# Kernel optimization log

Hardware: AMD Instinct MI355X
Metric: run time of the kernel (lower is better)

Reference implementation:

```python
import jax, jax.numpy as jnp
import numpy as np

D = 768           # input_dim == slot_dim
H, DH = 8, 64     # encoder attention heads / head dim (x-transformers defaults)
INNER = 4 * D     # ff_mult=4 GLU inner dim
EPS = 1e-8
N_ITERS = 3
SCALE = D ** -0.5


def _ln(x, g, b):
    m = jnp.mean(x, axis=-1, keepdims=True)
    v = jnp.var(x, axis=-1, keepdims=True)
    return (x - m) / jnp.sqrt(v + 1e-5) * g + b


def setup_inputs() -> dict:
    key = jax.random.key(0)
    ks = jax.random.split(key, 16)
    w = lambda i, shape, s=0.02: jax.random.normal(ks[i], shape, jnp.float32) * s
    return dict(
        x=jax.random.normal(ks[0], (32, 1024, D), jnp.float32),
        noise=jax.random.normal(ks[1], (32, 16, D), jnp.float32),
        init_mu=jax.random.normal(ks[2], (D,), jnp.float32),
        init_log_sigma=w(3, (D,), 0.05),
        Wk=w(4, (D, D)), Wv=w(5, (D, D)), Wq=w(6, (D, D)),
        ni_g=jnp.ones(D), ni_b=jnp.zeros(D),       # norm_input
        ns_g=jnp.ones(D), ns_b=jnp.zeros(D),       # norm_slots
        nica_g=jnp.ones(D), nica_b=jnp.zeros(D),   # norm_ica
        ln1_g=jnp.ones(D), ln1_b=jnp.zeros(D),     # encoder attn pre-norm
        Wq_a=w(7, (D, H * DH)), Wk_a=w(8, (D, H * DH)),
        Wv_a=w(9, (D, H * DH)), Wo_a=w(10, (H * DH, D)),
        ln2_g=jnp.ones(D), ln2_b=jnp.zeros(D),     # encoder ff pre-norm
        W1=w(11, (D, 2 * INNER)), W2=w(12, (INNER, D)),
        lnf_g=jnp.ones(D), lnf_b=jnp.zeros(D),     # encoder final norm
    )


def _inv_cross_attn(q, k, v):
    # softmax over the SLOT axis (dim i), then renormalize over keys j
    dots = jnp.einsum('bid,bjd->bij', q, k) * SCALE
    attn = jax.nn.softmax(dots, axis=1) + EPS
    attn = attn / jnp.sum(attn, axis=-1, keepdims=True)
    updates = jnp.einsum('bjd,bij->bid', v, attn)
    return updates, attn


def _encoder(h, ln1_g, ln1_b, Wq_a, Wk_a, Wv_a, Wo_a, ln2_g, ln2_b, W1, W2, lnf_g, lnf_b):
    b, n, _ = h.shape
    a = _ln(h, ln1_g, ln1_b)
    q = (a @ Wq_a).reshape(b, n, H, DH)
    k = (a @ Wk_a).reshape(b, n, H, DH)
    v = (a @ Wv_a).reshape(b, n, H, DH)
    scores = jnp.einsum('bihd,bjhd->bhij', q, k) * (DH ** -0.5)
    p = jax.nn.softmax(scores, axis=-1)
    o = jnp.einsum('bhij,bjhd->bihd', p, v).reshape(b, n, H * DH)
    h = h + o @ Wo_a
    f = _ln(h, ln2_g, ln2_b)
    u, g = jnp.split(f @ W1, 2, axis=-1)
    h = h + (u * jax.nn.silu(g)) @ W2
    return _ln(h, lnf_g, lnf_b)


def reference(x, noise, init_mu, init_log_sigma, Wk, Wv, Wq,
              ni_g, ni_b, ns_g, ns_b, nica_g, nica_b,
              ln1_g, ln1_b, Wq_a, Wk_a, Wv_a, Wo_a,
              ln2_g, ln2_b, W1, W2, lnf_g, lnf_b):
    xn = _ln(x, ni_g, ni_b)
    k = xn @ Wk
    v = xn @ Wv
    slots = init_mu + jnp.exp(init_log_sigma) * noise  # [b, n_slots, d]

    def step(slots):
        q = _ln(slots, ns_g, ns_b) @ Wq
        updates, attn = _inv_cross_attn(q, k, v)
        slots = _ln(slots + updates, nica_g, nica_b)
        slots = _encoder(slots, ln1_g, ln1_b, Wq_a, Wk_a, Wv_a, Wo_a,
                         ln2_g, ln2_b, W1, W2, lnf_g, lnf_b)
        return slots, attn

    for _ in range(N_ITERS):
        slots, _ = step(slots)
    slots, attn = step(slots)
    attn_map = jnp.transpose(attn, (0, 2, 1))  # b n hw -> b hw n
    return slots, attn_map
```

## Files before the change

### kernel.cpp

```cpp
#include <hip/hip_runtime.h>
#include <hip/hip_bf16.h>
#include <stdint.h>

typedef _Float16 f16;
typedef __attribute__((ext_vector_type(8))) _Float16 f16x8;
typedef __attribute__((ext_vector_type(4))) _Float16 f16x4;
typedef __attribute__((ext_vector_type(4))) float f32x4;

#define GLOBAL_AS __attribute__((address_space(1)))
#define LDS_AS __attribute__((address_space(3)))

#define D_DIM 768
#define NTOK 1024
#define NSLOT 16
#define NB 32
#define NTOT (NB*NTOK)
#define HDIM 512
#define INNER 3072
#define SCALE_D 0.03608439182435161f
#define SCALE_H 0.125f

template<int OUT>
__global__ __launch_bounds__(256) void mgemm64_k(
    const f16* __restrict__ A, const f16* __restrict__ Bt,
    void* __restrict__ Cout, int M, int N, int K, int Kc)
{
  __shared__ __align__(16) f16 As[64*256];
  __shared__ __align__(16) f16 Bs[64*256];
  const int tid = threadIdx.x;
  const int lane = tid & 63;
  const int wave = tid >> 6;
  const int m0 = blockIdx.x*64, n0 = blockIdx.y*64;
  const int kbeg = blockIdx.z * Kc;
  const int wm = (wave>>1)*32, wn = (wave&1)*32;
  const int quad = lane>>4, l16 = lane&15;

  const int sr = tid>>2;
  const int sc = (tid&3)*8;
  const f16* gA = A  + (size_t)(m0+sr)*K + kbeg + sc;
  const f16* gB = Bt + (size_t)(n0+sr)*K + kbeg + sc;
  LDS_AS f16* lA = (LDS_AS f16*)&As[(size_t)tid*8];
  LDS_AS f16* lB = (LDS_AS f16*)&Bs[(size_t)tid*8];

  const f16* fA0 = &As[(wm + l16)*32 + quad*8];
  const f16* fB0 = &Bs[(wn + l16)*32 + quad*8];

  f32x4 acc[2][2] = {};

  for (int k0 = 0; k0 < Kc; k0 += 256){
    #pragma unroll
    for (int p=0;p<8;++p){
      __builtin_amdgcn_global_load_lds((const GLOBAL_AS void*)(gA + k0 + p*32),
                                       (LDS_AS void*)(lA + (size_t)p*2048), 16, 0, 0);
      __builtin_amdgcn_global_load_lds((const GLOBAL_AS void*)(gB + k0 + p*32),
                                       (LDS_AS void*)(lB + (size_t)p*2048), 16, 0, 0);
    }
    __syncthreads();
    #pragma unroll
    for (int p=0;p<8;++p){
      f16x8 a0 = *(const f16x8*)(fA0 + p*2048);
      f16x8 a1 = *(const f16x8*)(fA0 + p*2048 + 16*32);
      f16x8 b0 = *(const f16x8*)(fB0 + p*2048);
      f16x8 b1 = *(const f16x8*)(fB0 + p*2048 + 16*32);
      acc[0][0] = __builtin_amdgcn_mfma_f32_16x16x32_f16(a0,b0,acc[0][0],0,0,0);
      acc[0][1] = __builtin_amdgcn_mfma_f32_16x16x32_f16(a0,b1,acc[0][1],0,0,0);
      acc[1][0] = __builtin_amdgcn_mfma_f32_16x16x32_f16(a1,b0,acc[1][0],0,0,0);
      acc[1][1] = __builtin_amdgcn_mfma_f32_16x16x32_f16(a1,b1,acc[1][1],0,0,0);
    }
    __syncthreads();
  }
  #pragma unroll
  for (int mt=0;mt<2;++mt){
    #pragma unroll
    for (int nt=0;nt<2;++nt){
      int gm = m0 + wm + mt*16 + quad*4;
      int gn = n0 + wn + nt*16 + l16;
      #pragma unroll
      for (int r=0;r<4;++r){
        float c = acc[mt][nt][r];
        size_t idx = (size_t)(gm+r)*N + gn;
        if (OUT==0)      ((float*)Cout)[idx] = c;
        else if (OUT==1) ((f16*)Cout)[idx] = (f16)c;
        else             atomicAdd(&((float*)Cout)[idx], c);
      }
    }
  }
}

__global__ __launch_bounds__(256) void w1glu_k(
    const f16* __restrict__ A, const f16* __restrict__ W1T,
    f16* __restrict__ act, int M)
{
  __shared__ __align__(16) f16 As[64*128];
  __shared__ __align__(16) f16 Bu[64*128];
  __shared__ __align__(16) f16 Bg[64*128];
  const int K = 768;
  const int tid = threadIdx.x;
  const int lane = tid & 63;
  const int wave = tid >> 6;
  const int m0 = blockIdx.x*64, n0 = blockIdx.y*64;
  const int wm = (wave>>1)*32, wn = (wave&1)*32;
  const int quad = lane>>4, l16 = lane&15;

  const int sr = tid>>2;
  const int sc = (tid&3)*8;
  const f16* gA  = A   + (size_t)(m0+sr)*K + sc;
  const f16* gBu = W1T + (size_t)(n0+sr)*K + sc;
  const f16* gBg = W1T + (size_t)(3072+n0+sr)*K + sc;
  LDS_AS f16* lA  = (LDS_AS f16*)&As[(size_t)tid*8];
  LDS_AS f16* lBu = (LDS_AS f16*)&Bu[(size_t)tid*8];
  LDS_AS f16* lBg = (LDS_AS f16*)&Bg[(size_t)tid*8];

  const f16* fA0 = &As[(wm + l16)*32 + quad*8];
  const f16* fU0 = &Bu[(wn + l16)*32 + quad*8];
  const f16* fG0 = &Bg[(wn + l16)*32 + quad*8];

  f32x4 accU[2][2] = {};
  f32x4 accG[2][2] = {};

  for (int k0 = 0; k0 < K; k0 += 128){
    #pragma unroll
    for (int p=0;p<4;++p){
      __builtin_amdgcn_global_load_lds((const GLOBAL_AS void*)(gA  + k0 + p*32),
                                       (LDS_AS void*)(lA  + (size_t)p*2048), 16, 0, 0);
      __builtin_amdgcn_global_load_lds((const GLOBAL_AS void*)(gBu + k0 + p*32),
                                       (LDS_AS void*)(lBu + (size_t)p*2048), 16, 0, 0);
      __builtin_amdgcn_global_load_lds((const GLOBAL_AS void*)(gBg + k0 + p*32),
                                       (LDS_AS void*)(lBg + (size_t)p*2048), 16, 0, 0);
    }
    __syncthreads();
    #pragma unroll
    for (int p=0;p<4;++p){
      f16x8 a0 = *(const f16x8*)(fA0 + p*2048);
      f16x8 a1 = *(const f16x8*)(fA0 + p*2048 + 16*32);
      f16x8 u0 = *(const f16x8*)(fU0 + p*2048);
      f16x8 u1 = *(const f16x8*)(fU0 + p*2048 + 16*32);
      f16x8 g0 = *(const f16x8*)(fG0 + p*2048);
      f16x8 g1 = *(const f16x8*)(fG0 + p*2048 + 16*32);
      accU[0][0] = __builtin_amdgcn_mfma_f32_16x16x32_f16(a0,u0,accU[0][0],0,0,0);
      accU[0][1] = __builtin_amdgcn_mfma_f32_16x16x32_f16(a0,u1,accU[0][1],0,0,0);
      accU[1][0] = __builtin_amdgcn_mfma_f32_16x16x32_f16(a1,u0,accU[1][0],0,0,0);
      accU[1][1] = __builtin_amdgcn_mfma_f32_16x16x32_f16(a1,u1,accU[1][1],0,0,0);
      accG[0][0] = __builtin_amdgcn_mfma_f32_16x16x32_f16(a0,g0,accG[0][0],0,0,0);
      accG[0][1] = __builtin_amdgcn_mfma_f32_16x16x32_f16(a0,g1,accG[0][1],0,0,0);
      accG[1][0] = __builtin_amdgcn_mfma_f32_16x16x32_f16(a1,g0,accG[1][0],0,0,0);
      accG[1][1] = __builtin_amdgcn_mfma_f32_16x16x32_f16(a1,g1,accG[1][1],0,0,0);
    }
    __syncthreads();
  }
  #pragma unroll
  for (int mt=0;mt<2;++mt){
    #pragma unroll
    for (int nt=0;nt<2;++nt){
      int gm = m0 + wm + mt*16 + quad*4;
      int gn = n0 + wn + nt*16 + l16;
      #pragma unroll
      for (int r=0;r<4;++r){
        float u = accU[mt][nt][r];
        float g = accG[mt][nt][r];
        float sg = g / (1.0f + __expf(-g));
        act[(size_t)(gm+r)*INNER + gn] = (f16)(u*sg);
      }
    }
  }
}

__global__ __launch_bounds__(256) void dots_k(
    const f16* __restrict__ Q,
    const f16* __restrict__ Xn,
    f16* __restrict__ attn,
    float* __restrict__ rsPart)
{
  __shared__ __align__(16) f16 qf[16*768];
  __shared__ __align__(16) f16 ks[64*256];
  __shared__ float rpart[4][16];
  const int b = blockIdx.x, jt = blockIdx.y;
  const int tid = threadIdx.x;
  const int lane = tid & 63;
  const int w = tid >> 6;
  const int quad = lane>>4, l16 = lane&15;

  #pragma unroll
  for (int c=0;c<6;++c){
    int p = c*256 + tid;
    int ki = p >> 6, qd = (p >> 4) & 3, rw = p & 15;
    f16x8 v = *(const f16x8*)(Q + ((size_t)(b*NSLOT+rw))*D_DIM + ki*32 + qd*8);
    *(f16x8*)&qf[(size_t)p*8] = v;
  }

  const f16* gK = Xn + ((size_t)(b*NTOK + jt*64 + (tid>>2)))*D_DIM + (tid&3)*8;
  LDS_AS f16* lK = (LDS_AS f16*)&ks[(size_t)tid*8];

  f32x4 acc = {};
  for (int it=0; it<3; ++it){
    #pragma unroll
    for (int p=0;p<8;++p)
      __builtin_amdgcn_global_load_lds((const GLOBAL_AS void*)(gK + it*256 + p*32),
                                       (LDS_AS void*)(lK + (size_t)p*2048), 16, 0, 0);
    __syncthreads();
    #pragma unroll
    for (int p=0;p<8;++p){
      f16x8 a  = *(const f16x8*)&qf[(((size_t)(it*8+p)*4 + quad)*16 + l16)*8];
      f16x8 bf = *(const f16x8*)&ks[(size_t)p*2048 + (w*16+l16)*32 + quad*8];
      acc = __builtin_amdgcn_mfma_f32_16x16x32_f16(a, bf, acc, 0, 0, 0);
    }
    __syncthreads();
  }

  float v0 = acc[0]*SCALE_D, v1 = acc[1]*SCALE_D, v2 = acc[2]*SCALE_D, v3 = acc[3]*SCALE_D;
  float mx = fmaxf(fmaxf(v0,v1), fmaxf(v2,v3));
  mx = fmaxf(mx, __shfl_xor(mx, 16));
  mx = fmaxf(mx, __shfl_xor(mx, 32));
  float e0 = __expf(v0-mx), e1 = __expf(v1-mx), e2 = __expf(v2-mx), e3 = __expf(v3-mx);
  float s = e0+e1+e2+e3;
  s += __shfl_xor(s, 16);
  s += __shfl_xor(s, 32);
  float inv = 1.0f/s;
  float a0 = e0*inv + 1e-8f, a1 = e1*inv + 1e-8f, a2 = e2*inv + 1e-8f, a3 = e3*inv + 1e-8f;

  int jcol = jt*64 + w*16 + l16;
  int ibase = b*NSLOT + quad*4;
  attn[(size_t)(ibase+0)*NTOK + jcol] = (f16)a0;
  attn[(size_t)(ibase+1)*NTOK + jcol] = (f16)a1;
  attn[(size_t)(ibase+2)*NTOK + jcol] = (f16)a2;
  attn[(size_t)(ibase+3)*NTOK + jcol] = (f16)a3;

  float t0=a0, t1=a1, t2=a2, t3=a3;
  #pragma unroll
  for (int m=1;m<16;m<<=1){
    t0 += __shfl_xor(t0, m);
    t1 += __shfl_xor(t1, m);
    t2 += __shfl_xor(t2, m);
    t3 += __shfl_xor(t3, m);
  }
  if (l16 == 0){
    rpart[w][quad*4+0] = t0;
    rpart[w][quad*4+1] = t1;
    rpart[w][quad*4+2] = t2;
    rpart[w][quad*4+3] = t3;
  }
  __syncthreads();
  if (tid < 16){
    float ss = rpart[0][tid] + rpart[1][tid] + rpart[2][tid] + rpart[3][tid];
    rsPart[(size_t)((b*16 + jt)<<4) + tid] = ss;
  }
}

__global__ __launch_bounds__(256) void attnv_k(
    const f16* __restrict__ attn,
    const float* __restrict__ rsPart,
    const f16* __restrict__ XnT,
    f16* __restrict__ t_out)
{
  __shared__ __align__(16) f16 Asl[16*256];
  __shared__ __align__(16) f16 Bsl[64*256];
  __shared__ float rsum[16];
  const int b = blockIdx.x, d0 = blockIdx.y*64;
  const int tid = threadIdx.x;
  const int lane = tid & 63;
  const int w = tid >> 6;
  const int quad = lane>>4, l16 = lane&15;

  if (tid < 16){
    float s = 0.f;
    #pragma unroll
    for (int jt=0;jt<16;++jt) s += rsPart[(size_t)((b*16 + jt)<<4) + tid];
    rsum[tid] = s;
  }

  const int pa = tid>>6, ta = tid&63;
  const f16* gA = attn + ((size_t)(b*NSLOT + (ta>>2)))*NTOK + (ta&3)*8;
  const f16* gB = XnT + ((size_t)(d0 + (tid>>2)))*NTOT + b*NTOK + (tid&3)*8;
  LDS_AS f16* lB = (LDS_AS f16*)&Bsl[(size_t)tid*8];

  f32x4 acc = {};
  for (int it=0; it<4; ++it){
    #pragma unroll
    for (int q=0;q<2;++q){
      int pq = pa*2 + q;
      __builtin_amdgcn_global_load_lds((const GLOBAL_AS void*)(gA + it*256 + pq*32),
                                       (LDS_AS void*)((LDS_AS f16*)&Asl[(size_t)pq*512 + ta*8]), 16, 0, 0);
    }
    #pragma unroll
    for (int p=0;p<8;++p)
      __builtin_amdgcn_global_load_lds((const GLOBAL_AS void*)(gB + it*256 + p*32),
                                       (LDS_AS void*)(lB + (size_t)p*2048), 16, 0, 0);
    __syncthreads();
    #pragma unroll
    for (int p=0;p<8;++p){
      f16x8 a  = *(const f16x8*)&Asl[(size_t)p*512 + l16*32 + quad*8];
      f16x8 bf = *(const f16x8*)&Bsl[(size_t)p*2048 + (w*16+l16)*32 + quad*8];
      acc = __builtin_amdgcn_mfma_f32_16x16x32_f16(a, bf, acc, 0, 0, 0);
    }
    __syncthreads();
  }
  int dcol = d0 + w*16 + l16;
  #pragma unroll
  for (int r=0;r<4;++r){
    int i = quad*4 + r;
    t_out[(size_t)(b*NSLOT + i)*D_DIM + dcol] = (f16)(acc[r] / rsum[i]);
  }
}

__global__ __launch_bounds__(256) void lnw_k(
    const float* __restrict__ X,
    const float* __restrict__ g, const float* __restrict__ bb,
    f16* __restrict__ out)
{
  const int lane = threadIdx.x & 63;
  const size_t row = (size_t)blockIdx.x*4 + (threadIdx.x>>6);
  const float* x = X + row*D_DIM;
  float4 v[3]; float s=0.f, ss=0.f;
  #pragma unroll
  for (int t=0;t<3;++t){
    v[t] = *(const float4*)(x + lane*4 + t*256);
    s  += v[t].x+v[t].y+v[t].z+v[t].w;
    ss += v[t].x*v[t].x+v[t].y*v[t].y+v[t].z*v[t].z+v[t].w*v[t].w;
  }
  #pragma unroll
  for (int m=1;m<64;m<<=1){ s += __shfl_xor(s,m); ss += __shfl_xor(ss,m); }
  float mean = s*(1.0f/768.0f);
  float inv  = rsqrtf(ss*(1.0f/768.0f) - mean*mean + 1e-5f);
  #pragma unroll
  for (int t=0;t<3;++t){
    int c0 = lane*4 + t*256;
    float4 gg = *(const float4*)(g + c0);
    float4 bv = *(const float4*)(bb + c0);
    f16x4 h4;
    h4.x = (f16)((v[t].x-mean)*inv*gg.x + bv.x);
    h4.y = (f16)((v[t].y-mean)*inv*gg.y + bv.y);
    h4.z = (f16)((v[t].z-mean)*inv*gg.z + bv.z);
    h4.w = (f16)((v[t].w-mean)*inv*gg.w + bv.w);
    *(f16x4*)(out + row*D_DIM + c0) = h4;
  }
}

template<bool ADD>
__global__ __launch_bounds__(256) void lnlnw_k(
    const float* __restrict__ X, const float* __restrict__ X2,
    const float* __restrict__ g1, const float* __restrict__ b1,
    const float* __restrict__ g2, const float* __restrict__ b2,
    float* __restrict__ out1, f16* __restrict__ out2)
{
  const int lane = threadIdx.x & 63;
  const size_t row = (size_t)blockIdx.x*4 + (threadIdx.x>>6);
  const float* x = X + row*D_DIM;
  const float* x2 = X2 + row*D_DIM;
  float4 v[3]; float s=0.f, ss=0.f;
  #pragma unroll
  for (int t=0;t<3;++t){
    int c0 = lane*4 + t*256;
    float4 a = *(const float4*)(x + c0);
    if (ADD){
      float4 b = *(const float4*)(x2 + c0);
      a.x+=b.x; a.y+=b.y; a.z+=b.z; a.w+=b.w;
    }
    v[t]=a;
    s  += v[t].x+v[t].y+v[t].z+v[t].w;
    ss += v[t].x*v[t].x+v[t].y*v[t].y+v[t].z*v[t].z+v[t].w*v[t].w;
  }
  #pragma unroll
  for (int m=1;m<64;m<<=1){ s += __shfl_xor(s,m); ss += __shfl_xor(ss,m); }
  float mean = s*(1.0f/768.0f);
  float inv  = rsqrtf(ss*(1.0f/768.0f) - mean*mean + 1e-5f);
  float y[3][4]; float s2=0.f, ss2=0.f;
  #pragma unroll
  for (int t=0;t<3;++t){
    int c0 = lane*4 + t*256;
    float4 gg = *(const float4*)(g1 + c0);
    float4 bv = *(const float4*)(b1 + c0);
    y[t][0] = (v[t].x-mean)*inv*gg.x + bv.x;
    y[t][1] = (v[t].y-mean)*inv*gg.y + bv.y;
    y[t][2] = (v[t].z-mean)*inv*gg.z + bv.z;
    y[t][3] = (v[t].w-mean)*inv*gg.w + bv.w;
    float4 o = { y[t][0], y[t][1], y[t][2], y[t][3] };
    *(float4*)(out1 + row*D_DIM + c0) = o;
    s2  += y[t][0]+y[t][1]+y[t][2]+y[t][3];
    ss2 += y[t][0]*y[t][0]+y[t][1]*y[t][1]+y[t][2]*y[t][2]+y[t][3]*y[t][3];
  }
  #pragma unroll
  for (int m=1;m<64;m<<=1){ s2 += __shfl_xor(s2,m); ss2 += __shfl_xor(ss2,m); }
  float mean2 = s2*(1.0f/768.0f);
  float inv2  = rsqrtf(ss2*(1.0f/768.0f) - mean2*mean2 + 1e-5f);
  #pragma unroll
  for (int t=0;t<3;++t){
    int c0 = lane*4 + t*256;
    float4 gg = *(const float4*)(g2 + c0);
    float4 bv = *(const float4*)(b2 + c0);
    f16x4 h4;
    h4.x = (f16)((y[t][0]-mean2)*inv2*gg.x + bv.x);
    h4.y = (f16)((y[t][1]-mean2)*inv2*gg.y + bv.y);
    h4.z = (f16)((y[t][2]-mean2)*inv2*gg.z + bv.z);
    h4.w = (f16)((y[t][3]-mean2)*inv2*gg.w + bv.w);
    *(f16x4*)(out2 + row*D_DIM + c0) = h4;
  }
}

__global__ __launch_bounds__(256) void slotsinit_k(
    const float* __restrict__ noise, const float* __restrict__ mu,
    const float* __restrict__ ls,
    const float* __restrict__ nsg, const float* __restrict__ nsb,
    float* __restrict__ slots, f16* __restrict__ tmp2)
{
  const int lane = threadIdx.x & 63;
  const size_t row = (size_t)blockIdx.x*4 + (threadIdx.x>>6);
  float4 v[3]; float s=0.f, ss=0.f;
  #pragma unroll
  for (int t=0;t<3;++t){
    int c0 = lane*4 + t*256;
    float4 nz = *(const float4*)(noise + row*D_DIM + c0);
    float4 m4 = *(const float4*)(mu + c0);
    float4 l4 = *(const float4*)(ls + c0);
    v[t].x = m4.x + __expf(l4.x)*nz.x;
    v[t].y = m4.y + __expf(l4.y)*nz.y;
    v[t].z = m4.z + __expf(l4.z)*nz.z;
    v[t].w = m4.w + __expf(l4.w)*nz.w;
    *(float4*)(slots + row*D_DIM + c0) = v[t];
    s  += v[t].x+v[t].y+v[t].z+v[t].w;
    ss += v[t].x*v[t].x+v[t].y*v[t].y+v[t].z*v[t].z+v[t].w*v[t].w;
  }
  #pragma unroll
  for (int m=1;m<64;m<<=1){ s += __shfl_xor(s,m); ss += __shfl_xor(ss,m); }
  float mean = s*(1.0f/768.0f);
  float inv  = rsqrtf(ss*(1.0f/768.0f) - mean*mean + 1e-5f);
  #pragma unroll
  for (int t=0;t<3;++t){
    int c0 = lane*4 + t*256;
    float4 gg = *(const float4*)(nsg + c0);
    float4 bv = *(const float4*)(nsb + c0);
    f16x4 h4;
    h4.x = (f16)((v[t].x-mean)*inv*gg.x + bv.x);
    h4.y = (f16)((v[t].y-mean)*inv*gg.y + bv.y);
    h4.z = (f16)((v[t].z-mean)*inv*gg.z + bv.z);
    h4.w = (f16)((v[t].w-mean)*inv*gg.w + bv.w);
    *(f16x4*)(tmp2 + row*D_DIM + c0) = h4;
  }
}

__global__ __launch_bounds__(256) void encattn_k(
    const f16* __restrict__ QA, const f16* __restrict__ KA,
    const f16* __restrict__ VA, int QSTR,
    f16* __restrict__ O)
{
  __shared__ float qs[16][68], ks[16][68], vs[16][68], ps[16][20];
  const int b = blockIdx.x, h = blockIdx.y;
  const int tid = threadIdx.x;
  {
    int i = tid>>4, dd=(tid&15)*4;
    size_t base = ((size_t)(b*NSLOT+i))*QSTR + h*64 + dd;
    f16x4 uq = *(const f16x4*)(QA + base);
    f16x4 uk = *(const f16x4*)(KA + base);
    f16x4 uv = *(const f16x4*)(VA + base);
    float4 fq = { (float)uq.x, (float)uq.y, (float)uq.z, (float)uq.w };
    float4 fk = { (float)uk.x, (float)uk.y, (float)uk.z, (float)uk.w };
    float4 fv = { (float)uv.x, (float)uv.y, (float)uv.z, (float)uv.w };
    *(float4*)&qs[i][dd]=fq; *(float4*)&ks[i][dd]=fk; *(float4*)&vs[i][dd]=fv;
  }
  __syncthreads();
  {
    int i = tid>>4, j = tid&15;
    float s=0.f;
    #pragma unroll 8
    for (int d=0; d<64; ++d) s += qs[i][d]*ks[j][d];
    ps[i][j] = s*SCALE_H;
  }
  __syncthreads();
  if (tid < 16){
    int i = tid;
    float mx=-1e30f;
    #pragma unroll
    for (int j=0;j<16;++j) mx = fmaxf(mx, ps[i][j]);
    float sm=0.f;
    #pragma unroll
    for (int j=0;j<16;++j){ float e=__expf(ps[i][j]-mx); ps[i][j]=e; sm+=e; }
    float inv=1.0f/sm;
    #pragma unroll
    for (int j=0;j<16;++j) ps[i][j]*=inv;
  }
  __syncthreads();
  {
    int i = tid>>4, dq=(tid&15)*4;
    float a0=0,a1=0,a2=0,a3=0;
    #pragma unroll
    for (int j=0;j<16;++j){
      float p = ps[i][j];
      a0+=p*vs[j][dq+0]; a1+=p*vs[j][dq+1]; a2+=p*vs[j][dq+2]; a3+=p*vs[j][dq+3];
    }
    size_t base = ((size_t)(b*NSLOT+i))*HDIM + h*64 + dq;
    O[base+0]=(f16)a0; O[base+1]=(f16)a1; O[base+2]=(f16)a2; O[base+3]=(f16)a3;
  }
}

__global__ __launch_bounds__(256) void transp_k(
    const f16* __restrict__ in, f16* __restrict__ out, int R, int C)
{
  __shared__ f16 T[64][72];
  const int m0 = blockIdx.x*64, d0 = blockIdx.y*64;
  const int tid = threadIdx.x;
  {
    int r = tid>>2, c = (tid&3)*16;
    const f16* p = in + (size_t)(m0+r)*C + d0 + c;
    *(f16x8*)&T[r][c]   = *(const f16x8*)p;
    *(f16x8*)&T[r][c+8] = *(const f16x8*)(p+8);
  }
  __syncthreads();
  {
    int dd = tid>>2, mq = (tid&3)*16;
    f16 v[16];
    #pragma unroll
    for (int e=0;e<16;++e) v[e] = T[mq+e][dd];
    f16* p = out + (size_t)(d0+dd)*R + m0 + mq;
    *(f16x8*)p     = *(f16x8*)&v[0];
    *(f16x8*)(p+8) = *(f16x8*)&v[8];
  }
}

__global__ __launch_bounds__(256) void prep_k(
    const float* __restrict__ Wv,   const float* __restrict__ Wq_a,
    const float* __restrict__ Wk_a, const float* __restrict__ Wv_a,
    const float* __restrict__ Wo_a, const float* __restrict__ W1,
    const float* __restrict__ W2,   const float* __restrict__ Wk,
    const float* __restrict__ Wq,
    f16* __restrict__ WvT, f16* __restrict__ WqkvT, f16* __restrict__ WoaT,
    f16* __restrict__ W1T, f16* __restrict__ W2T,
    f16* __restrict__ Wkf, f16* __restrict__ Wqf)
{
  __shared__ float t[32][33];
  int bid = blockIdx.x;
  const float* src; f16* dst; int R, C; bool tr = true;
  if      (bid < 576)  {              src=Wv;   dst=WvT;             R=768;  C=768; }
  else if (bid < 960)  { bid-=576;    src=Wq_a; dst=WqkvT;           R=768;  C=512; }
  else if (bid < 1344) { bid-=960;    src=Wk_a; dst=WqkvT+512*768;   R=768;  C=512; }
  else if (bid < 1728) { bid-=1344;   src=Wv_a; dst=WqkvT+1024*768;  R=768;  C=512; }
  else if (bid < 2112) { bid-=1728;   src=Wo_a; dst=WoaT;            R=512;  C=768; }
  else if (bid < 6720) { bid-=2112;   src=W1;   dst=W1T;             R=768;  C=6144; }
  else if (bid < 9024) { bid-=6720;   src=W2;   dst=W2T;             R=3072; C=768; }
  else if (bid < 9600) { bid-=9024;   src=Wk;   dst=Wkf;             R=768;  C=768; tr=false; }
  else                 { bid-=9600;   src=Wq;   dst=Wqf;             R=768;  C=768; tr=false; }
  const int tpr = C/32;
  const int r0 = (bid / tpr)*32, c0 = (bid % tpr)*32;
  const int lc = threadIdx.x & 31, g8 = threadIdx.x >> 5;
  if (tr){
    #pragma unroll
    for (int s=0;s<4;++s){
      int r = g8*4 + s;
      t[r][lc] = src[(size_t)(r0+r)*C + c0+lc];
    }
    __syncthreads();
    #pragma unroll
    for (int s=0;s<4;++s){
      int c = g8*4 + s;
      dst[(size_t)(c0+c)*R + r0+lc] = (f16)t[lc][c];
    }
  } else {
    #pragma unroll
    for (int s=0;s<4;++s){
      int r = g8*4 + s;
      dst[(size_t)(r0+r)*C + c0+lc] = (f16)src[(size_t)(r0+r)*C + c0+lc];
    }
  }
}

__global__ __launch_bounds__(256) void attnout_k(
    const f16* __restrict__ attn, const float* __restrict__ rsPart,
    float* __restrict__ out)
{
  __shared__ float rsum[16];
  const int bid = blockIdx.x, tid = threadIdx.x;
  const int b = bid >> 6;
  if (tid < 16){
    float s = 0.f;
    #pragma unroll
    for (int jt=0;jt<16;++jt) s += rsPart[(size_t)((b*16+jt)<<4) + tid];
    rsum[tid] = s;
  }
  __syncthreads();
  int idx = bid*256 + tid;
  int i = idx & 15;
  int j = (idx >> 4) & 1023;
  out[idx] = (float)attn[((size_t)(b*NSLOT)+i)*NTOK + j] / rsum[i];
}

extern "C" void kernel_launch(void* const* d_in, const int* in_sizes, int n_in,
                              void* d_out, int out_size, void* d_ws, size_t ws_size,
                              hipStream_t stream) {
  const float* x        = (const float*)d_in[0];
  const float* noise    = (const float*)d_in[1];
  const float* init_mu  = (const float*)d_in[2];
  const float* init_ls  = (const float*)d_in[3];
  const float* Wk       = (const float*)d_in[4];
  const float* Wv       = (const float*)d_in[5];
  const float* Wq       = (const float*)d_in[6];
  const float* ni_g     = (const float*)d_in[7];
  const float* ni_b     = (const float*)d_in[8];
  const float* ns_g     = (const float*)d_in[9];
  const float* ns_b     = (const float*)d_in[10];
  const float* nica_g   = (const float*)d_in[11];
  const float* nica_b   = (const float*)d_in[12];
  const float* ln1_g    = (const float*)d_in[13];
  const float* ln1_b    = (const float*)d_in[14];
  const float* Wq_a     = (const float*)d_in[15];
  const float* Wk_a     = (const float*)d_in[16];
  const float* Wv_a     = (const float*)d_in[17];
  const float* Wo_a     = (const float*)d_in[18];
  const float* ln2_g    = (const float*)d_in[19];
  const float* ln2_b    = (const float*)d_in[20];
  const float* W1       = (const float*)d_in[21];
  const float* W2       = (const float*)d_in[22];
  const float* lnf_g    = (const float*)d_in[23];
  const float* lnf_b    = (const float*)d_in[24];

  char* w = (char*)d_ws;
  size_t off = 0;
  auto alloc = [&](size_t bytes)->char*{
    char* p = w + off; off += (bytes + 255) & ~(size_t)255; return p;
  };
  f16* xn_h  = (f16*)alloc((size_t)NTOT*D_DIM*2);
  f16* xnT_h = (f16*)alloc((size_t)D_DIM*NTOT*2);
  f16* Wkf   = (f16*)alloc((size_t)768*768*2);
  f16* Wqf   = (f16*)alloc((size_t)768*768*2);
  f16* BtQK  = (f16*)alloc((size_t)768*768*2);
  f16* WvT   = (f16*)alloc((size_t)768*768*2);
  f16* WqkvT = (f16*)alloc((size_t)1536*768*2);
  f16* WoaT  = (f16*)alloc((size_t)768*512*2);
  f16* W1T   = (f16*)alloc((size_t)6144*768*2);
  f16* W2T   = (f16*)alloc((size_t)768*3072*2);
  float* slots = (float*)alloc(512*768*4);
  float* hbuf  = (float*)alloc(512*768*4);
  float* upd   = (float*)alloc(512*768*4);
  f16* tmp_h  = (f16*)alloc(512*768*2);
  f16* tmp2_h = (f16*)alloc(512*768*2);
  f16* q_h    = (f16*)alloc(512*768*2);
  f16* t_h    = (f16*)alloc(512*768*2);
  f16* qkv_h  = (f16*)alloc((size_t)512*1536*2);
  f16* o_h    = (f16*)alloc(512*512*2);
  f16* act_h  = (f16*)alloc((size_t)512*3072*2);
  f16* attn_h = (f16*)alloc((size_t)NB*NSLOT*NTOK*2);
  float* rsPart = (float*)alloc((size_t)32*16*16*4);

  prep_k<<<10176, 256, 0, stream>>>(Wv, Wq_a, Wk_a, Wv_a, Wo_a, W1, W2, Wk, Wq,
                                    WvT, WqkvT, WoaT, W1T, W2T, Wkf, Wqf);

  mgemm64_k<1><<<dim3(12, 12, 1), 256, 0, stream>>>(Wkf, Wqf, BtQK, 768, 768, 768, 768);

  lnw_k<<<NTOT/4, 256, 0, stream>>>(x, ni_g, ni_b, xn_h);
  transp_k<<<dim3(NTOT/64, D_DIM/64), 256, 0, stream>>>(xn_h, xnT_h, NTOT, D_DIM);

  slotsinit_k<<<128, 256, 0, stream>>>(noise, init_mu, init_ls, ns_g, ns_b,
                                       slots, tmp2_h);

  for (int it=0; it<4; ++it){
    mgemm64_k<1><<<dim3(8, 12, 1), 256, 0, stream>>>(tmp2_h, BtQK, q_h, 512, 768, 768, 768);
    dots_k<<<dim3(NB, 16), 256, 0, stream>>>(q_h, xn_h, attn_h, rsPart);
    attnv_k<<<dim3(NB, 12), 256, 0, stream>>>(attn_h, rsPart, xnT_h, t_h);
    mgemm64_k<0><<<dim3(8, 12, 1), 256, 0, stream>>>(t_h, WvT, upd, 512, 768, 768, 768);
    lnlnw_k<true><<<128, 256, 0, stream>>>(slots, upd, nica_g, nica_b, ln1_g, ln1_b,
                                           hbuf, tmp_h);
    mgemm64_k<1><<<dim3(8, 24, 1), 256, 0, stream>>>(tmp_h, WqkvT, qkv_h, 512, 1536, 768, 768);
    encattn_k<<<dim3(NB, 8), 256, 0, stream>>>(qkv_h, qkv_h + 512, qkv_h + 1024, 1536, o_h);
    mgemm64_k<2><<<dim3(8, 12, 2), 256, 0, stream>>>(o_h, WoaT, hbuf, 512, 768, 512, 256);
    lnw_k<<<128, 256, 0, stream>>>(hbuf, ln2_g, ln2_b, tmp_h);
    w1glu_k<<<dim3(8, 48), 256, 0, stream>>>(tmp_h, W1T, act_h, 512);
    mgemm64_k<2><<<dim3(8, 12, 4), 256, 0, stream>>>(act_h, W2T, hbuf, 512, 768, 3072, 768);
    float* out1 = (it==3) ? (float*)d_out : slots;
    lnlnw_k<false><<<128, 256, 0, stream>>>(hbuf, nullptr, lnf_g, lnf_b, ns_g, ns_b,
                                            out1, tmp2_h);
  }

  attnout_k<<<NB*NTOK*NSLOT/256, 256, 0, stream>>>(attn_h, rsPart, (float*)d_out + 512*768);
}
```

Measured before the change: 625.8 us.

## Fuse per-iteration slot-attention pipeline into one cooperative persistent megakernel

Replaces the dozen per-iteration kernel launches (dots, attn·V, GEMMs, layer norms, encoder attention, GLU FFN, next-iteration Q projection) with one cooperative kernel. The stages run as grid-stride tile loops separated by grid.sync(). The aim is to remove launch overhead and inter-kernel gaps for these small 512-row workloads. The grid is sized from occupancy, assuming 256 CUs and capped at 512 blocks. If the cooperative launch fails, the original multi-kernel path is used. The trade-off is the cost of grid-wide barriers, plus lower parallelism in phases that have fewer tiles than blocks.

```diff
diff --git a/kernel.cpp b/kernel.cpp
--- a/kernel.cpp
+++ b/kernel.cpp
@@ -1,4 +1,5 @@
 #include <hip/hip_runtime.h>
+#include <hip/hip_cooperative_groups.h>
 #include <hip/hip_bf16.h>
 #include <stdint.h>
 
@@ -19,6 +20,7 @@
 #define INNER 3072
 #define SCALE_D 0.03608439182435161f
 #define SCALE_H 0.125f
+
 
 template<int OUT>
 __global__ __launch_bounds__(256) void mgemm64_k(
@@ -166,10 +168,8 @@
 }
 
 __global__ __launch_bounds__(256) void dots_k(
-    const f16* __restrict__ Q,
-    const f16* __restrict__ Xn,
-    f16* __restrict__ attn,
-    float* __restrict__ rsPart)
+    const f16* __restrict__ Q, const f16* __restrict__ Xn,
+    f16* __restrict__ attn, float* __restrict__ rsPart)
 {
   __shared__ __align__(16) f16 qf[16*768];
   __shared__ __align__(16) f16 ks[64*256];
@@ -247,10 +247,8 @@
 }
 
 __global__ __launch_bounds__(256) void attnv_k(
-    const f16* __restrict__ attn,
-    const float* __restrict__ rsPart,
-    const f16* __restrict__ XnT,
-    f16* __restrict__ t_out)
+    const f16* __restrict__ attn, const float* __restrict__ rsPart,
+    const f16* __restrict__ XnT, f16* __restrict__ t_out)
 {
   __shared__ __align__(16) f16 Asl[16*256];
   __shared__ __align__(16) f16 Bsl[64*256];
@@ -579,6 +577,461 @@
   int i = idx & 15;
   int j = (idx >> 4) & 1023;
   out[idx] = (float)attn[((size_t)(b*NSLOT)+i)*NTOK + j] / rsum[i];
+}
+
+
+struct MegaArgs {
+  const f16* q; const f16* xn; const f16* xnT;
+  f16* attn; float* rsPart; f16* t;
+  const f16* WvT; float* upd;
+  const float* slots; float* hbuf;
+  f16* tmp; f16* tmp2;
+  const f16* WqkvT; f16* qkv; f16* o;
+  const f16* WoaT; const f16* W1T; f16* act; const f16* W2T;
+  const f16* BtQK; f16* qnext; float* out1;
+  const float* nica_g; const float* nica_b;
+  const float* ln1_g;  const float* ln1_b;
+  const float* ln2_g;  const float* ln2_b;
+  const float* lnf_g;  const float* lnf_b;
+  const float* ns_g;   const float* ns_b;
+  int doQnext;
+};
+
+template<int OUT>
+__device__ __forceinline__ void gemm_tile(
+    const f16* __restrict__ A, const f16* __restrict__ Bt, void* __restrict__ Cout,
+    int N, int K, int m0, int n0, int kbeg, int Kc, char* smraw, int tid)
+{
+  f16* As = (f16*)smraw;
+  f16* Bs = (f16*)(smraw + 16384);
+  const int lane = tid & 63;
+  const int wave = tid >> 6;
+  const int wm = (wave>>1)*32, wn = (wave&1)*32;
+  const int quad = lane>>4, l16 = lane&15;
+  const int sr = tid>>2, sc = (tid&3)*8;
+  const f16* gA = A  + (size_t)(m0+sr)*K + kbeg + sc;
+  const f16* gB = Bt + (size_t)(n0+sr)*K + kbeg + sc;
+  LDS_AS f16* lA = (LDS_AS f16*)&As[(size_t)tid*8];
+  LDS_AS f16* lB = (LDS_AS f16*)&Bs[(size_t)tid*8];
+  const f16* fA0 = &As[(wm + l16)*32 + quad*8];
+  const f16* fB0 = &Bs[(wn + l16)*32 + quad*8];
+  f32x4 acc[2][2] = {};
+  for (int k0 = 0; k0 < Kc; k0 += 128){
+    #pragma unroll
+    for (int p=0;p<4;++p){
+      __builtin_amdgcn_global_load_lds((const GLOBAL_AS void*)(gA + k0 + p*32),
+                                       (LDS_AS void*)(lA + (size_t)p*2048), 16, 0, 0);
+      __builtin_amdgcn_global_load_lds((const GLOBAL_AS void*)(gB + k0 + p*32),
+                                       (LDS_AS void*)(lB + (size_t)p*2048), 16, 0, 0);
+    }
+    __syncthreads();
+    #pragma unroll
+    for (int p=0;p<4;++p){
+      f16x8 a0 = *(const f16x8*)(fA0 + p*2048);
+      f16x8 a1 = *(const f16x8*)(fA0 + p*2048 + 16*32);
+      f16x8 b0 = *(const f16x8*)(fB0 + p*2048);
+      f16x8 b1 = *(const f16x8*)(fB0 + p*2048 + 16*32);
+      acc[0][0] = __builtin_amdgcn_mfma_f32_16x16x32_f16(a0,b0,acc[0][0],0,0,0);
+      acc[0][1] = __builtin_amdgcn_mfma_f32_16x16x32_f16(a0,b1,acc[0][1],0,0,0);
+      acc[1][0] = __builtin_amdgcn_mfma_f32_16x16x32_f16(a1,b0,acc[1][0],0,0,0);
+      acc[1][1] = __builtin_amdgcn_mfma_f32_16x16x32_f16(a1,b1,acc[1][1],0,0,0);
+    }
+    __syncthreads();
+  }
+  #pragma unroll
+  for (int mt=0;mt<2;++mt){
+    #pragma unroll
+    for (int nt=0;nt<2;++nt){
+      int gm = m0 + wm + mt*16 + quad*4;
+      int gn = n0 + wn + nt*16 + l16;
+      #pragma unroll
+      for (int r=0;r<4;++r){
+        float c = acc[mt][nt][r];
+        size_t idx = (size_t)(gm+r)*N + gn;
+        if (OUT==0)      ((float*)Cout)[idx] = c;
+        else if (OUT==1) ((f16*)Cout)[idx] = (f16)c;
+        else             atomicAdd(&((float*)Cout)[idx], c);
+      }
+    }
+  }
+}
+
+template<bool ADD>
+__device__ __forceinline__ void lnln_rows(
+    const float* __restrict__ X, const float* __restrict__ X2,
+    const float* __restrict__ g1, const float* __restrict__ b1,
+    const float* __restrict__ g2, const float* __restrict__ b2,
+    float* __restrict__ out1, f16* __restrict__ out2, int gidx, int tid)
+{
+  const int lane = tid & 63;
+  const size_t row = (size_t)gidx*4 + (tid>>6);
+  const size_t ro = row*D_DIM;
+  float4 v[3]; float s=0.f, ss=0.f;
+  #pragma unroll
+  for (int t=0;t<3;++t){
+    int c0 = lane*4 + t*256;
+    float4 a = *(const float4*)(X + ro + c0);
+    if (ADD){
+      float4 b = *(const float4*)(X2 + ro + c0);
+      a.x+=b.x; a.y+=b.y; a.z+=b.z; a.w+=b.w;
+    }
+    v[t]=a;
+    s  += a.x+a.y+a.z+a.w;
+    ss += a.x*a.x+a.y*a.y+a.z*a.z+a.w*a.w;
+  }
+  #pragma unroll
+  for (int m=1;m<64;m<<=1){ s += __shfl_xor(s,m); ss += __shfl_xor(ss,m); }
+  float mean = s*(1.0f/768.0f);
+  float inv  = rsqrtf(ss*(1.0f/768.0f) - mean*mean + 1e-5f);
+  float y[3][4]; float s2=0.f, ss2=0.f;
+  #pragma unroll
+  for (int t=0;t<3;++t){
+    int c0 = lane*4 + t*256;
+    float4 gg = *(const float4*)(g1 + c0);
+    float4 bv = *(const float4*)(b1 + c0);
+    y[t][0] = (v[t].x-mean)*inv*gg.x + bv.x;
+    y[t][1] = (v[t].y-mean)*inv*gg.y + bv.y;
+    y[t][2] = (v[t].z-mean)*inv*gg.z + bv.z;
+    y[t][3] = (v[t].w-mean)*inv*gg.w + bv.w;
+    float4 o = { y[t][0], y[t][1], y[t][2], y[t][3] };
+    *(float4*)(out1 + ro + c0) = o;
+    s2  += y[t][0]+y[t][1]+y[t][2]+y[t][3];
+    ss2 += y[t][0]*y[t][0]+y[t][1]*y[t][1]+y[t][2]*y[t][2]+y[t][3]*y[t][3];
+  }
+  #pragma unroll
+  for (int m=1;m<64;m<<=1){ s2 += __shfl_xor(s2,m); ss2 += __shfl_xor(ss2,m); }
+  float mean2 = s2*(1.0f/768.0f);
+  float inv2  = rsqrtf(ss2*(1.0f/768.0f) - mean2*mean2 + 1e-5f);
+  #pragma unroll
+  for (int t=0;t<3;++t){
+    int c0 = lane*4 + t*256;
+    float4 gg = *(const float4*)(g2 + c0);
+    float4 bv = *(const float4*)(b2 + c0);
+    f16x4 h4;
+    h4.x = (f16)((y[t][0]-mean2)*inv2*gg.x + bv.x);
+    h4.y = (f16)((y[t][1]-mean2)*inv2*gg.y + bv.y);
+    h4.z = (f16)((y[t][2]-mean2)*inv2*gg.z + bv.z);
+    h4.w = (f16)((y[t][3]-mean2)*inv2*gg.w + bv.w);
+    *(f16x4*)(out2 + ro + c0) = h4;
+  }
+}
+
+__device__ __forceinline__ void ln_rows(
+    const float* __restrict__ X,
+    const float* __restrict__ g, const float* __restrict__ bb,
+    f16* __restrict__ out, int gidx, int tid)
+{
+  const int lane = tid & 63;
+  const size_t row = (size_t)gidx*4 + (tid>>6);
+  const float* x = X + row*D_DIM;
+  float4 v[3]; float s=0.f, ss=0.f;
+  #pragma unroll
+  for (int t=0;t<3;++t){
+    v[t] = *(const float4*)(x + lane*4 + t*256);
+    s  += v[t].x+v[t].y+v[t].z+v[t].w;
+    ss += v[t].x*v[t].x+v[t].y*v[t].y+v[t].z*v[t].z+v[t].w*v[t].w;
+  }
+  #pragma unroll
+  for (int m=1;m<64;m<<=1){ s += __shfl_xor(s,m); ss += __shfl_xor(ss,m); }
+  float mean = s*(1.0f/768.0f);
+  float inv  = rsqrtf(ss*(1.0f/768.0f) - mean*mean + 1e-5f);
+  #pragma unroll
+  for (int t=0;t<3;++t){
+    int c0 = lane*4 + t*256;
+    float4 gg = *(const float4*)(g + c0);
+    float4 bv = *(const float4*)(bb + c0);
+    f16x4 h4;
+    h4.x = (f16)((v[t].x-mean)*inv*gg.x + bv.x);
+    h4.y = (f16)((v[t].y-mean)*inv*gg.y + bv.y);
+    h4.z = (f16)((v[t].z-mean)*inv*gg.z + bv.z);
+    h4.w = (f16)((v[t].w-mean)*inv*gg.w + bv.w);
+    *(f16x4*)(out + row*D_DIM + c0) = h4;
+  }
+}
+
+__global__ __launch_bounds__(256) void mega_k(MegaArgs a)
+{
+  __shared__ __align__(16) char smraw[57600];
+  cooperative_groups::grid_group grid = cooperative_groups::this_grid();
+  const int tid = threadIdx.x;
+  const int lane = tid & 63;
+  const int w = tid >> 6;
+  const int quad = lane>>4, l16 = lane&15;
+  const int NBLK = gridDim.x;
+
+  for (int tile = blockIdx.x; tile < 512; tile += NBLK){
+    const int b = tile & 31, jt = tile >> 5;
+    f16* qf = (f16*)smraw;
+    f16* ks = (f16*)(smraw + 24576);
+    float* rpart = (float*)(smraw + 57344);
+    __syncthreads();
+    #pragma unroll
+    for (int c=0;c<6;++c){
+      int p = c*256 + tid;
+      int ki = p >> 6, qd = (p >> 4) & 3, rw = p & 15;
+      f16x8 v = *(const f16x8*)(a.q + ((size_t)(b*NSLOT+rw))*D_DIM + ki*32 + qd*8);
+      *(f16x8*)&qf[(size_t)p*8] = v;
+    }
+    const f16* gK = a.xn + ((size_t)(b*NTOK + jt*64 + (tid>>2)))*D_DIM + (tid&3)*8;
+    LDS_AS f16* lK = (LDS_AS f16*)&ks[(size_t)tid*8];
+    f32x4 acc = {};
+    for (int it=0; it<3; ++it){
+      #pragma unroll
+      for (int p=0;p<8;++p)
+        __builtin_amdgcn_global_load_lds((const GLOBAL_AS void*)(gK + it*256 + p*32),
+                                         (LDS_AS void*)(lK + (size_t)p*2048), 16, 0, 0);
+      __syncthreads();
+      #pragma unroll
+      for (int p=0;p<8;++p){
+        f16x8 av = *(const f16x8*)&qf[(((size_t)(it*8+p)*4 + quad)*16 + l16)*8];
+        f16x8 bf = *(const f16x8*)&ks[(size_t)p*2048 + (w*16+l16)*32 + quad*8];
+        acc = __builtin_amdgcn_mfma_f32_16x16x32_f16(av, bf, acc, 0, 0, 0);
+      }
+      __syncthreads();
+    }
+    float v0 = acc[0]*SCALE_D, v1 = acc[1]*SCALE_D, v2 = acc[2]*SCALE_D, v3 = acc[3]*SCALE_D;
+    float mx = fmaxf(fmaxf(v0,v1), fmaxf(v2,v3));
+    mx = fmaxf(mx, __shfl_xor(mx, 16));
+    mx = fmaxf(mx, __shfl_xor(mx, 32));
+    float e0 = __expf(v0-mx), e1 = __expf(v1-mx), e2 = __expf(v2-mx), e3 = __expf(v3-mx);
+    float s = e0+e1+e2+e3;
+    s += __shfl_xor(s, 16);
+    s += __shfl_xor(s, 32);
+    float inv = 1.0f/s;
+    float a0 = e0*inv + 1e-8f, a1 = e1*inv + 1e-8f, a2 = e2*inv + 1e-8f, a3 = e3*inv + 1e-8f;
+    int jcol = jt*64 + w*16 + l16;
+    int ibase = b*NSLOT + quad*4;
+    a.attn[(size_t)(ibase+0)*NTOK + jcol] = (f16)a0;
+    a.attn[(size_t)(ibase+1)*NTOK + jcol] = (f16)a1;
+    a.attn[(size_t)(ibase+2)*NTOK + jcol] = (f16)a2;
+    a.attn[(size_t)(ibase+3)*NTOK + jcol] = (f16)a3;
+    float t0=a0, t1=a1, t2=a2, t3=a3;
+    #pragma unroll
+    for (int m=1;m<16;m<<=1){
+      t0 += __shfl_xor(t0, m);
+      t1 += __shfl_xor(t1, m);
+      t2 += __shfl_xor(t2, m);
+      t3 += __shfl_xor(t3, m);
+    }
+    if (l16 == 0){
+      rpart[w*16 + quad*4+0] = t0;
+      rpart[w*16 + quad*4+1] = t1;
+      rpart[w*16 + quad*4+2] = t2;
+      rpart[w*16 + quad*4+3] = t3;
+    }
+    __syncthreads();
+    if (tid < 16){
+      float ssum = rpart[0*16+tid] + rpart[1*16+tid] + rpart[2*16+tid] + rpart[3*16+tid];
+      a.rsPart[(size_t)((b*16 + jt)<<4) + tid] = ssum;
+    }
+  }
+  grid.sync();
+
+  for (int tile = blockIdx.x; tile < 384; tile += NBLK){
+    const int b = tile & 31, d0 = (tile >> 5)*64;
+    f16* Asl = (f16*)smraw;
+    f16* Bsl = (f16*)(smraw + 8192);
+    float* rsum = (float*)(smraw + 40960);
+    __syncthreads();
+    if (tid < 16){
+      float s = 0.f;
+      #pragma unroll
+      for (int jt=0;jt<16;++jt) s += a.rsPart[(size_t)((b*16 + jt)<<4) + tid];
+      rsum[tid] = s;
+    }
+    const int pa = tid>>6, ta = tid&63;
+    const f16* gA = a.attn + ((size_t)(b*NSLOT + (ta>>2)))*NTOK + (ta&3)*8;
+    const f16* gB = a.xnT + ((size_t)(d0 + (tid>>2)))*NTOT + b*NTOK + (tid&3)*8;
+    LDS_AS f16* lB = (LDS_AS f16*)&Bsl[(size_t)tid*8];
+    f32x4 acc = {};
+    for (int it=0; it<4; ++it){
+      #pragma unroll
+      for (int q=0;q<2;++q){
+        int pq = pa*2 + q;
+        __builtin_amdgcn_global_load_lds((const GLOBAL_AS void*)(gA + it*256 + pq*32),
+                                         (LDS_AS void*)((LDS_AS f16*)&Asl[(size_t)pq*512 + ta*8]), 16, 0, 0);
+      }
+      #pragma unroll
+      for (int p=0;p<8;++p)
+        __builtin_amdgcn_global_load_lds((const GLOBAL_AS void*)(gB + it*256 + p*32),
+                                         (LDS_AS void*)(lB + (size_t)p*2048), 16, 0, 0);
+      __syncthreads();
+      #pragma unroll
+      for (int p=0;p<8;++p){
+        f16x8 av = *(const f16x8*)&Asl[(size_t)p*512 + l16*32 + quad*8];
+        f16x8 bf = *(const f16x8*)&Bsl[(size_t)p*2048 + (w*16+l16)*32 + quad*8];
+        acc = __builtin_amdgcn_mfma_f32_16x16x32_f16(av, bf, acc, 0, 0, 0);
+      }
+      __syncthreads();
+    }
+    int dcol = d0 + w*16 + l16;
+    #pragma unroll
+    for (int r=0;r<4;++r){
+      int i = quad*4 + r;
+      a.t[(size_t)(b*NSLOT + i)*D_DIM + dcol] = (f16)(acc[r] / rsum[i]);
+    }
+  }
+  grid.sync();
+
+  for (int tile = blockIdx.x; tile < 96; tile += NBLK)
+    gemm_tile<0>(a.t, a.WvT, a.upd, 768, 768, (tile&7)*64, (tile>>3)*64, 0, 768, smraw, tid);
+  grid.sync();
+
+  for (int g = blockIdx.x; g < 128; g += NBLK)
+    lnln_rows<true>(a.slots, a.upd, a.nica_g, a.nica_b, a.ln1_g, a.ln1_b,
+                    a.hbuf, a.tmp, g, tid);
+  grid.sync();
+
+  for (int tile = blockIdx.x; tile < 192; tile += NBLK)
+    gemm_tile<1>(a.tmp, a.WqkvT, a.qkv, 1536, 768, (tile&7)*64, (tile>>3)*64, 0, 768, smraw, tid);
+  grid.sync();
+
+  for (int tile = blockIdx.x; tile < 256; tile += NBLK){
+    const int b = tile & 31, h = tile >> 5;
+    float* qs = (float*)smraw;
+    float* ks2 = (float*)(smraw + 4352);
+    float* vs = (float*)(smraw + 8704);
+    float* ps = (float*)(smraw + 13056);
+    __syncthreads();
+    {
+      int i = tid>>4, dd=(tid&15)*4;
+      size_t base = ((size_t)(b*NSLOT+i))*1536 + h*64 + dd;
+      f16x4 uq = *(const f16x4*)(a.qkv + base);
+      f16x4 uk = *(const f16x4*)(a.qkv + 512 + base);
+      f16x4 uv = *(const f16x4*)(a.qkv + 1024 + base);
+      float4 fq = { (float)uq.x, (float)uq.y, (float)uq.z, (float)uq.w };
+      float4 fk = { (float)uk.x, (float)uk.y, (float)uk.z, (float)uk.w };
+      float4 fv = { (float)uv.x, (float)uv.y, (float)uv.z, (float)uv.w };
+      *(float4*)&qs[i*68+dd]=fq; *(float4*)&ks2[i*68+dd]=fk; *(float4*)&vs[i*68+dd]=fv;
+    }
+    __syncthreads();
+    {
+      int i = tid>>4, j = tid&15;
+      float s=0.f;
+      #pragma unroll 8
+      for (int d=0; d<64; ++d) s += qs[i*68+d]*ks2[j*68+d];
+      ps[i*20+j] = s*SCALE_H;
+    }
+    __syncthreads();
+    if (tid < 16){
+      int i = tid;
+      float mx=-1e30f;
+      #pragma unroll
+      for (int j=0;j<16;++j) mx = fmaxf(mx, ps[i*20+j]);
+      float sm=0.f;
+      #pragma unroll
+      for (int j=0;j<16;++j){ float e=__expf(ps[i*20+j]-mx); ps[i*20+j]=e; sm+=e; }
+      float inv=1.0f/sm;
+      #pragma unroll
+      for (int j=0;j<16;++j) ps[i*20+j]*=inv;
+    }
+    __syncthreads();
+    {
+      int i = tid>>4, dq=(tid&15)*4;
+      float a0=0,a1=0,a2=0,a3=0;
+      #pragma unroll
+      for (int j=0;j<16;++j){
+        float p = ps[i*20+j];
+        a0+=p*vs[j*68+dq+0]; a1+=p*vs[j*68+dq+1]; a2+=p*vs[j*68+dq+2]; a3+=p*vs[j*68+dq+3];
+      }
+      size_t base = ((size_t)(b*NSLOT+i))*HDIM + h*64 + dq;
+      a.o[base+0]=(f16)a0; a.o[base+1]=(f16)a1; a.o[base+2]=(f16)a2; a.o[base+3]=(f16)a3;
+    }
+  }
+  grid.sync();
+
+  for (int tile = blockIdx.x; tile < 192; tile += NBLK){
+    int z = tile/96, r = tile%96;
+    gemm_tile<2>(a.o, a.WoaT, a.hbuf, 768, 512, (r&7)*64, (r>>3)*64, z*256, 256, smraw, tid);
+  }
+  grid.sync();
+
+  for (int g = blockIdx.x; g < 128; g += NBLK)
+    ln_rows(a.hbuf, a.ln2_g, a.ln2_b, a.tmp, g, tid);
+  grid.sync();
+
+  for (int tile = blockIdx.x; tile < 384; tile += NBLK){
+    const int m0 = (tile&7)*64, n0 = (tile>>3)*64;
+    f16* As = (f16*)smraw;
+    f16* Bu = (f16*)(smraw + 16384);
+    f16* Bg = (f16*)(smraw + 32768);
+    const int wave = w;
+    const int wm = (wave>>1)*32, wn = (wave&1)*32;
+    const int sr = tid>>2, sc = (tid&3)*8;
+    const f16* gA  = a.tmp + (size_t)(m0+sr)*768 + sc;
+    const f16* gBu = a.W1T + (size_t)(n0+sr)*768 + sc;
+    const f16* gBg = a.W1T + (size_t)(3072+n0+sr)*768 + sc;
+    LDS_AS f16* lA  = (LDS_AS f16*)&As[(size_t)tid*8];
+    LDS_AS f16* lBu = (LDS_AS f16*)&Bu[(size_t)tid*8];
+    LDS_AS f16* lBg = (LDS_AS f16*)&Bg[(size_t)tid*8];
+    const f16* fA0 = &As[(wm + l16)*32 + quad*8];
+    const f16* fU0 = &Bu[(wn + l16)*32 + quad*8];
+    const f16* fG0 = &Bg[(wn + l16)*32 + quad*8];
+    f32x4 accU[2][2] = {};
+    f32x4 accG[2][2] = {};
+    for (int k0 = 0; k0 < 768; k0 += 128){
+      #pragma unroll
+      for (int p=0;p<4;++p){
+        __builtin_amdgcn_global_load_lds((const GLOBAL_AS void*)(gA  + k0 + p*32),
+                                         (LDS_AS void*)(lA  + (size_t)p*2048), 16, 0, 0);
+        __builtin_amdgcn_global_load_lds((const GLOBAL_AS void*)(gBu + k0 + p*32),
+                                         (LDS_AS void*)(lBu + (size_t)p*2048), 16, 0, 0);
+        __builtin_amdgcn_global_load_lds((const GLOBAL_AS void*)(gBg + k0 + p*32),
+                                         (LDS_AS void*)(lBg + (size_t)p*2048), 16, 0, 0);
+      }
+      __syncthreads();
+      #pragma unroll
+      for (int p=0;p<4;++p){
+        f16x8 a0 = *(const f16x8*)(fA0 + p*2048);
+        f16x8 a1 = *(const f16x8*)(fA0 + p*2048 + 16*32);
+        f16x8 u0 = *(const f16x8*)(fU0 + p*2048);
+        f16x8 u1 = *(const f16x8*)(fU0 + p*2048 + 16*32);
+        f16x8 g0 = *(const f16x8*)(fG0 + p*2048);
+        f16x8 g1 = *(const f16x8*)(fG0 + p*2048 + 16*32);
+        accU[0][0] = __builtin_amdgcn_mfma_f32_16x16x32_f16(a0,u0,accU[0][0],0,0,0);
+        accU[0][1] = __builtin_amdgcn_mfma_f32_16x16x32_f16(a0,u1,accU[0][1],0,0,0);
+        accU[1][0] = __builtin_amdgcn_mfma_f32_16x16x32_f16(a1,u0,accU[1][0],0,0,0);
+        accU[1][1] = __builtin_amdgcn_mfma_f32_16x16x32_f16(a1,u1,accU[1][1],0,0,0);
+        accG[0][0] = __builtin_amdgcn_mfma_f32_16x16x32_f16(a0,g0,accG[0][0],0,0,0);
+        accG[0][1] = __builtin_amdgcn_mfma_f32_16x16x32_f16(a0,g1,accG[0][1],0,0,0);
+        accG[1][0] = __builtin_amdgcn_mfma_f32_16x16x32_f16(a1,g0,accG[1][0],0,0,0);
+        accG[1][1] = __builtin_amdgcn_mfma_f32_16x16x32_f16(a1,g1,accG[1][1],0,0,0);
+      }
+      __syncthreads();
+    }
+    #pragma unroll
+    for (int mt=0;mt<2;++mt){
+      #pragma unroll
+      for (int nt=0;nt<2;++nt){
+        int gm = m0 + wm + mt*16 + quad*4;
+        int gn = n0 + wn + nt*16 + l16;
+        #pragma unroll
+        for (int r=0;r<4;++r){
+          float u = accU[mt][nt][r];
+          float g = accG[mt][nt][r];
+          float sg = g / (1.0f + __expf(-g));
+          a.act[(size_t)(gm+r)*INNER + gn] = (f16)(u*sg);
+        }
+      }
+    }
+  }
+  grid.sync();
+
+  for (int tile = blockIdx.x; tile < 384; tile += NBLK){
+    int z = tile/96, r = tile%96;
+    gemm_tile<2>(a.act, a.W2T, a.hbuf, 768, 3072, (r&7)*64, (r>>3)*64, z*768, 768, smraw, tid);
+  }
+  grid.sync();
+
+  for (int g = blockIdx.x; g < 128; g += NBLK)
+    lnln_rows<false>(a.hbuf, nullptr, a.lnf_g, a.lnf_b, a.ns_g, a.ns_b,
+                     a.out1, a.tmp2, g, tid);
+
+  if (a.doQnext){
+    grid.sync();
+    for (int tile = blockIdx.x; tile < 96; tile += NBLK)
+      gemm_tile<1>(a.tmp2, a.BtQK, a.qnext, 768, 768, (tile&7)*64, (tile>>3)*64, 0, 768, smraw, tid);
+  }
 }
 
 extern "C" void kernel_launch(void* const* d_in, const int* in_sizes, int n_in,
@@ -640,31 +1093,65 @@
 
   prep_k<<<10176, 256, 0, stream>>>(Wv, Wq_a, Wk_a, Wv_a, Wo_a, W1, W2, Wk, Wq,
                                     WvT, WqkvT, WoaT, W1T, W2T, Wkf, Wqf);
-
   mgemm64_k<1><<<dim3(12, 12, 1), 256, 0, stream>>>(Wkf, Wqf, BtQK, 768, 768, 768, 768);
-
   lnw_k<<<NTOT/4, 256, 0, stream>>>(x, ni_g, ni_b, xn_h);
   transp_k<<<dim3(NTOT/64, D_DIM/64), 256, 0, stream>>>(xn_h, xnT_h, NTOT, D_DIM);
-
   slotsinit_k<<<128, 256, 0, stream>>>(noise, init_mu, init_ls, ns_g, ns_b,
                                        slots, tmp2_h);
+  mgemm64_k<1><<<dim3(8, 12, 1), 256, 0, stream>>>(tmp2_h, BtQK, q_h, 512, 768, 768, 768);
+
+  int occ = 0;
+  bool coop = (hipOccupancyMaxActiveBlocksPerMultiprocessor(&occ, mega_k, 256, 0) == hipSuccess)
+              && (occ >= 1);
+  int nblk = 0;
+  if (coop){
+    nblk = occ * 256;
+    if (nblk > 512) nblk = 512;
+  }
 
   for (int it=0; it<4; ++it){
-    mgemm64_k<1><<<dim3(8, 12, 1), 256, 0, stream>>>(tmp2_h, BtQK, q_h, 512, 768, 768, 768);
-    dots_k<<<dim3(NB, 16), 256, 0, stream>>>(q_h, xn_h, attn_h, rsPart);
-    attnv_k<<<dim3(NB, 12), 256, 0, stream>>>(attn_h, rsPart, xnT_h, t_h);
-    mgemm64_k<0><<<dim3(8, 12, 1), 256, 0, stream>>>(t_h, WvT, upd, 512, 768, 768, 768);
-    lnlnw_k<true><<<128, 256, 0, stream>>>(slots, upd, nica_g, nica_b, ln1_g, ln1_b,
-                                           hbuf, tmp_h);
-    mgemm64_k<1><<<dim3(8, 24, 1), 256, 0, stream>>>(tmp_h, WqkvT, qkv_h, 512, 1536, 768, 768);
-    encattn_k<<<dim3(NB, 8), 256, 0, stream>>>(qkv_h, qkv_h + 512, qkv_h + 1024, 1536, o_h);
-    mgemm64_k<2><<<dim3(8, 12, 2), 256, 0, stream>>>(o_h, WoaT, hbuf, 512, 768, 512, 256);
-    lnw_k<<<128, 256, 0, stream>>>(hbuf, ln2_g, ln2_b, tmp_h);
-    w1glu_k<<<dim3(8, 48), 256, 0, stream>>>(tmp_h, W1T, act_h, 512);
-    mgemm64_k<2><<<dim3(8, 12, 4), 256, 0, stream>>>(act_h, W2T, hbuf, 512, 768, 3072, 768);
-    float* out1 = (it==3) ? (float*)d_out : slots;
-    lnlnw_k<false><<<128, 256, 0, stream>>>(hbuf, nullptr, lnf_g, lnf_b, ns_g, ns_b,
-                                            out1, tmp2_h);
+    bool ran_coop = false;
+    if (coop){
+      MegaArgs ma;
+      ma.q = q_h; ma.xn = xn_h; ma.xnT = xnT_h;
+      ma.attn = attn_h; ma.rsPart = rsPart; ma.t = t_h;
+      ma.WvT = WvT; ma.upd = upd;
+      ma.slots = slots; ma.hbuf = hbuf;
+      ma.tmp = tmp_h; ma.tmp2 = tmp2_h;
+      ma.WqkvT = WqkvT; ma.qkv = qkv_h; ma.o = o_h;
+      ma.WoaT = WoaT; ma.W1T = W1T; ma.act = act_h; ma.W2T = W2T;
+      ma.BtQK = BtQK; ma.qnext = q_h;
+      ma.out1 = (it==3) ? (float*)d_out : slots;
+      ma.nica_g = nica_g; ma.nica_b = nica_b;
+      ma.ln1_g = ln1_g;   ma.ln1_b = ln1_b;
+      ma.ln2_g = ln2_g;   ma.ln2_b = ln2_b;
+      ma.lnf_g = lnf_g;   ma.lnf_b = lnf_b;
+      ma.ns_g = ns_g;     ma.ns_b = ns_b;
+      ma.doQnext = (it<3) ? 1 : 0;
+      void* kp[] = { &ma };
+      hipError_t err = hipLaunchCooperativeKernel((const void*)mega_k,
+                                                  dim3(nblk), dim3(256), kp, 0, stream);
+      if (err == hipSuccess) ran_coop = true;
+      else coop = false;
+    }
+    if (!ran_coop){
+      if (it > 0)
+        mgemm64_k<1><<<dim3(8, 12, 1), 256, 0, stream>>>(tmp2_h, BtQK, q_h, 512, 768, 768, 768);
+      dots_k<<<dim3(NB, 16), 256, 0, stream>>>(q_h, xn_h, attn_h, rsPart);
+      attnv_k<<<dim3(NB, 12), 256, 0, stream>>>(attn_h, rsPart, xnT_h, t_h);
+      mgemm64_k<0><<<dim3(8, 12, 1), 256, 0, stream>>>(t_h, WvT, upd, 512, 768, 768, 768);
+      lnlnw_k<true><<<128, 256, 0, stream>>>(slots, upd, nica_g, nica_b, ln1_g, ln1_b,
+                                             hbuf, tmp_h);
+      mgemm64_k<1><<<dim3(8, 24, 1), 256, 0, stream>>>(tmp_h, WqkvT, qkv_h, 512, 1536, 768, 768);
+      encattn_k<<<dim3(NB, 8), 256, 0, stream>>>(qkv_h, qkv_h + 512, qkv_h + 1024, 1536, o_h);
+      mgemm64_k<2><<<dim3(8, 12, 2), 256, 0, stream>>>(o_h, WoaT, hbuf, 512, 768, 512, 256);
+      lnw_k<<<128, 256, 0, stream>>>(hbuf, ln2_g, ln2_b, tmp_h);
+      w1glu_k<<<dim3(8, 48), 256, 0, stream>>>(tmp_h, W1T, act_h, 512);
+      mgemm64_k<2><<<dim3(8, 12, 4), 256, 0, stream>>>(act_h, W2T, hbuf, 512, 768, 3072, 768);
+      float* out1 = (it==3) ? (float*)d_out : slots;
+      lnlnw_k<false><<<128, 256, 0, stream>>>(hbuf, nullptr, lnf_g, lnf_b, ns_g, ns_b,
+                                              out1, tmp2_h);
+    }
   }
 
   attnout_k<<<NB*NTOK*NSLOT/256, 256, 0, stream>>>(attn_h, rsPart, (float*)d_out + 512*768);
```

New measurement: 1.948 ms. 211% more time.
